# Optimization experiments

Measured on AMD Instinct MI355X. Metric: run time of the kernel, lower is better.

The kernel has to match this reference:

```python
import jax, jax.numpy as jnp
import numpy as np

D_MODEL = 1024
N_HEADS = 16
D_HEAD = D_MODEL // N_HEADS
N_INS = 3
RANK = 16
EPS = 1e-5


def gelu1p(x):
    # gelu1p feature map: 1 + GELU(x) (positive-ish feature map for linear attention)
    return 1.0 + jax.nn.gelu(x, approximate=False)


def setup_inputs() -> dict:
    key = jax.random.key(0)
    ks = jax.random.split(key, 16)
    B, T = 4, 8192
    x = jax.random.normal(ks[0], (B, T, D_MODEL), dtype=jnp.float32)
    pad_mask = jnp.ones((B, T), dtype=bool)
    s = 1.0 / np.sqrt(D_MODEL)
    wq = jax.random.normal(ks[1], (D_MODEL, D_MODEL), jnp.float32) * s
    wk = jax.random.normal(ks[2], (D_MODEL, D_MODEL), jnp.float32) * s
    wv = jax.random.normal(ks[3], (D_MODEL, D_MODEL), jnp.float32) * s
    wo = jax.random.normal(ks[4], (D_MODEL, D_MODEL), jnp.float32) * s
    sr = 1.0 / np.sqrt(RANK)
    # LoRA weights stacked over insertion points: down (n_ins, rank, d), up (n_ins, d, rank)
    # NOTE: original zero-inits 'up'; we use small random values so LoRA path is exercised.
    def lora(k1, k2):
        return (jax.random.normal(k1, (N_INS, RANK, D_MODEL), jnp.float32) * s,
                jax.random.normal(k2, (N_INS, D_MODEL, RANK), jnp.float32) * sr * 0.01)
    lqd, lqu = lora(ks[5], ks[6])
    lkd, lku = lora(ks[7], ks[8])
    lvd, lvu = lora(ks[9], ks[10])
    lod, lou = lora(ks[11], ks[12])
    return {"x": x, "pad_mask": pad_mask, "insertion_idx": 1,
            "wq": wq, "wk": wk, "wv": wv, "wo": wo,
            "lqd": lqd, "lqu": lqu, "lkd": lkd, "lku": lku,
            "lvd": lvd, "lvu": lvu, "lod": lod, "lou": lou}


def _proj(x, w, down, up):
    # base linear (no bias) + LoRA: x @ w.T + (x @ down.T) @ up.T
    return x @ w.T + (x @ down.T) @ up.T


def reference(x, pad_mask, insertion_idx, wq, wk, wv, wo,
              lqd, lqu, lkd, lku, lvd, lvu, lod, lou):
    B, T, D = x.shape
    i = insertion_idx
    q = _proj(x, wq, lqd[i], lqu[i])
    k = _proj(x, wk, lkd[i], lku[i])
    v = _proj(x, wv, lvd[i], lvu[i])
    # (B, T, H, dh) -> (B, H, T, dh)
    q = q.reshape(B, T, N_HEADS, D_HEAD).transpose(0, 2, 1, 3)
    k = k.reshape(B, T, N_HEADS, D_HEAD).transpose(0, 2, 1, 3)
    v = v.reshape(B, T, N_HEADS, D_HEAD).transpose(0, 2, 1, 3)
    q = gelu1p(q)
    k = gelu1p(k)
    m = pad_mask[:, None, :, None].astype(k.dtype)  # (B,1,T,1)
    k = k * m
    v = v * m
    context = jnp.einsum('bhtd,bhte->bhde', k, v)  # (B,H,dh,dh)
    z = k.sum(axis=-2)                              # (B,H,dh)
    num = jnp.einsum('bhtd,bhde->bhte', q, context)
    den = jnp.einsum('bhtd,bhd->bht', q, z)
    out = num / (den[..., None] + EPS)
    out = out.transpose(0, 2, 1, 3).reshape(B, T, D)
    out = _proj(out, wo, lod[i], lou[i])
    return out
```

## Files before the change

kernel.cpp:

```cpp
#include <hip/hip_runtime.h>
#include <hip/hip_bf16.h>

typedef unsigned short u16;
typedef __attribute__((ext_vector_type(8))) short short8;
typedef __attribute__((ext_vector_type(4))) float f32x4;
typedef __attribute__((ext_vector_type(4))) unsigned short us4;
typedef __attribute__((ext_vector_type(8))) unsigned short us8;

__device__ __forceinline__ u16 f2bf(float f) {
  unsigned int u = __float_as_uint(f);
  u += 0x7fffu + ((u >> 16) & 1u);
  return (u16)(u >> 16);
}
__device__ __forceinline__ float bf2f(u16 h) {
  return __uint_as_float(((unsigned int)h) << 16);
}
__device__ __forceinline__ float gelu1p_f(float x) {
  const float z  = x * 0.7071067811865475f;
  const float az = __builtin_fabsf(z);
  const float t  = __builtin_amdgcn_rcpf(__builtin_fmaf(0.3275911f, az, 1.0f));
  float pl = __builtin_fmaf(1.061405429f, t, -1.453152027f);
  pl = __builtin_fmaf(pl, t, 1.421413741f);
  pl = __builtin_fmaf(pl, t, -0.284496736f);
  pl = __builtin_fmaf(pl, t, 0.254829592f);
  pl = pl * t;
  const float e = __builtin_amdgcn_exp2f(-az * az * 1.4426950408889634f);
  float erfa = __builtin_fmaf(-pl, e, 1.0f);
  erfa = __builtin_copysignf(erfa, z);
  return __builtin_fmaf(x, 0.5f * (1.0f + erfa), 1.0f);
}
__device__ __forceinline__ void gll16(const void* g, void* l) {
  __builtin_amdgcn_global_load_lds(
      (const __attribute__((address_space(1))) unsigned int*)g,
      (__attribute__((address_space(3))) unsigned int*)l, 16, 0, 0);
}
#define FENCE() __builtin_amdgcn_sched_barrier(0)
#define BARRIER() __builtin_amdgcn_s_barrier()
#define LGKM0() do { asm volatile("s_waitcnt lgkmcnt(0)" ::: "memory"); FENCE(); } while (0)
#define VMCNT4() do { asm volatile("s_waitcnt vmcnt(4)" ::: "memory"); FENCE(); } while (0)
#define MFMA16(a, b, c) __builtin_amdgcn_mfma_f32_16x16x32_bf16(a, b, c, 0, 0, 0)

__global__ __launch_bounds__(256)
void build_weff(const float* __restrict__ wq, const float* __restrict__ wk,
                const float* __restrict__ wv, const float* __restrict__ wo,
                const float* __restrict__ lqd, const float* __restrict__ lqu,
                const float* __restrict__ lkd, const float* __restrict__ lku,
                const float* __restrict__ lvd, const float* __restrict__ lvu,
                const float* __restrict__ lod, const float* __restrict__ lou,
                const int* __restrict__ idxp,
                u16* __restrict__ wqkv, u16* __restrict__ wout) {
  const int blk = blockIdx.x;
  const int p = blk >> 10;
  const int n = blk & 1023;
  const int i = *idxp;
  const float* W  = (p == 0) ? wq  : (p == 1) ? wk  : (p == 2) ? wv  : wo;
  const float* Dn = ((p == 0) ? lqd : (p == 1) ? lkd : (p == 2) ? lvd : lod) + (size_t)i * 16 * 1024;
  const float* Up = ((p == 0) ? lqu : (p == 1) ? lku : (p == 2) ? lvu : lou) + (size_t)i * 1024 * 16;

  float up[16];
#pragma unroll
  for (int r = 0; r < 16; ++r) up[r] = Up[n * 16 + r];

  const int k0 = threadIdx.x << 2;
  f32x4 acc = *(const f32x4*)&W[(size_t)n * 1024 + k0];
#pragma unroll
  for (int r = 0; r < 16; ++r) {
    const f32x4 d = *(const f32x4*)&Dn[r * 1024 + k0];
#pragma unroll
    for (int j = 0; j < 4; ++j) acc[j] = __builtin_fmaf(up[r], d[j], acc[j]);
  }
  us4 o;
#pragma unroll
  for (int j = 0; j < 4; ++j) o[j] = f2bf(acc[j]);
  if (p < 3) *(us4*)&wqkv[(size_t)(p * 1024 + n) * 1024 + k0] = o;
  else       *(us4*)&wout[(size_t)n * 1024 + k0] = o;
}

__global__ void xcast(const float* __restrict__ x, u16* __restrict__ xb) {
  const size_t i = ((size_t)blockIdx.x * 256 + threadIdx.x) * 8;
  f32x4 a = *(const f32x4*)(x + i);
  f32x4 b = *(const f32x4*)(x + i + 4);
  us8 o;
#pragma unroll
  for (int j = 0; j < 4; ++j) { o[j] = f2bf(a[j]); o[j + 4] = f2bf(b[j]); }
  *(us8*)(xb + i) = o;
}

template <int MODE>
__global__ __launch_bounds__(512, 2)
void gemm8p(const u16* __restrict__ A, const u16* __restrict__ Bw,
            u16* __restrict__ qb, u16* __restrict__ kbuf, u16* __restrict__ vbuf,
            float* __restrict__ outf, const int* __restrict__ mask, int nbx) {
  const int nwg = gridDim.x;
  const int cpx = nwg >> 3;
  const int wg0 = blockIdx.x;
  const int swz = (wg0 & 7) * cpx + (wg0 >> 3);
  const int bx = swz % nbx;
  const int by = swz / nbx;
  const int row0 = by << 8, col0 = bx << 8;
  const int tid = threadIdx.x, lane = tid & 63, w = tid >> 6;
  const int wr = w >> 2, wc = w & 3;

  __shared__ __align__(16) u16 lds[2][2][2][8192];

  const int srow = (w << 4) + (lane & 15);
  const int scol = (lane >> 4) << 3;
  const u16* pA = A  + (size_t)(row0 + srow) * 1024 + scol;
  const u16* pB = Bw + (size_t)(col0 + srow) * 1024 + scol;

  auto stA = [&](int bb, int h, int ts) {
    const u16* s = pA + h * 131072 + ts * 64;
    u16* d = &lds[bb][0][h][((w << 7) + lane) << 3];
    gll16(s, d); gll16(s + 32, d + 512);
  };
  auto stB = [&](int bb, int h, int ts) {
    const u16* s = pB + h * 131072 + ts * 64;
    u16* d = &lds[bb][1][h][((w << 7) + lane) << 3];
    gll16(s, d); gll16(s + 32, d + 512);
  };
  auto LDA = [&](int bb, int m, int kk) {
    return *(const short8*)&lds[bb][0][wr][((((m << 1) | kk) << 6) | lane) << 3];
  };
  auto LDB = [&](int bb, int n, int kk) {
    const int nn = ((wc & 1) << 2) | n;
    return *(const short8*)&lds[bb][1][wc >> 1][((((nn << 1) | kk) << 6) | lane) << 3];
  };

  f32x4 acc[8][4] = {};
  short8 af[4][2], bfv[4][2];

  stA(0, 0, 0); stB(0, 0, 0); stA(0, 1, 0); stB(0, 1, 0);
  stB(1, 0, 1); stA(1, 0, 1);
  VMCNT4();
  BARRIER();

  auto tile = [&](int BUF, int t) {
    const int t1 = (t + 1 < 16) ? t + 1 : 15;
    const int t2 = (t + 2 < 16) ? t + 2 : 15;
#pragma unroll
    for (int m = 0; m < 4; ++m) { af[m][0] = LDA(BUF, m, 0); af[m][1] = LDA(BUF, m, 1); }
#pragma unroll
    for (int n = 0; n < 2; ++n) { bfv[n][0] = LDB(BUF, n, 0); bfv[n][1] = LDB(BUF, n, 1); }
    stA(BUF ^ 1, 1, t1);
    FENCE(); BARRIER(); LGKM0();
    __builtin_amdgcn_s_setprio(1);
#pragma unroll
    for (int m = 0; m < 4; ++m)
#pragma unroll
      for (int n = 0; n < 2; ++n) {
        acc[m][n] = MFMA16(af[m][0], bfv[n][0], acc[m][n]);
        acc[m][n] = MFMA16(af[m][1], bfv[n][1], acc[m][n]);
      }
    __builtin_amdgcn_s_setprio(0);
    FENCE(); BARRIER();
#pragma unroll
    for (int n = 2; n < 4; ++n) { bfv[n][0] = LDB(BUF, n, 0); bfv[n][1] = LDB(BUF, n, 1); }
    stB(BUF ^ 1, 1, t1);
    FENCE(); BARRIER(); LGKM0();
    __builtin_amdgcn_s_setprio(1);
#pragma unroll
    for (int m = 0; m < 4; ++m)
#pragma unroll
      for (int n = 2; n < 4; ++n) {
        acc[m][n] = MFMA16(af[m][0], bfv[n][0], acc[m][n]);
        acc[m][n] = MFMA16(af[m][1], bfv[n][1], acc[m][n]);
      }
    __builtin_amdgcn_s_setprio(0);
    FENCE(); BARRIER();
#pragma unroll
    for (int m = 0; m < 4; ++m) { af[m][0] = LDA(BUF, 4 + m, 0); af[m][1] = LDA(BUF, 4 + m, 1); }
    stB(BUF, 0, t2);
    FENCE(); BARRIER(); LGKM0();
    __builtin_amdgcn_s_setprio(1);
#pragma unroll
    for (int m = 0; m < 4; ++m)
#pragma unroll
      for (int n = 2; n < 4; ++n) {
        acc[4 + m][n] = MFMA16(af[m][0], bfv[n][0], acc[4 + m][n]);
        acc[4 + m][n] = MFMA16(af[m][1], bfv[n][1], acc[4 + m][n]);
      }
    __builtin_amdgcn_s_setprio(0);
    FENCE(); BARRIER();
    stA(BUF, 0, t2);
    FENCE(); BARRIER();
    __builtin_amdgcn_s_setprio(1);
#pragma unroll
    for (int m = 0; m < 4; ++m)
#pragma unroll
      for (int n = 0; n < 2; ++n) {
        acc[4 + m][n] = MFMA16(af[m][0], bfv[n][0], acc[4 + m][n]);
        acc[4 + m][n] = MFMA16(af[m][1], bfv[n][1], acc[4 + m][n]);
      }
    __builtin_amdgcn_s_setprio(0);
    FENCE();
    VMCNT4();
    BARRIER();
  };

#pragma unroll
  for (int it = 0; it < 8; ++it) { tile(0, 2 * it); tile(1, 2 * it + 1); }

  if (MODE == 0) {
    const int cw = col0 + (wc << 6);
    const int p = cw >> 10;
    u16* dst = (p == 0) ? qb : (p == 1) ? kbuf : vbuf;
    const int cc0 = (cw & 1023) + (lane & 15);
#pragma unroll
    for (int m = 0; m < 8; ++m) {
      const int r0 = row0 + (wr << 7) + (m << 4) + ((lane >> 4) << 2);
#pragma unroll
      for (int j = 0; j < 4; ++j) {
        const int r = r0 + j;
        const float mv = (p == 0) ? 1.0f : ((mask[r] != 0) ? 1.0f : 0.0f);
#pragma unroll
        for (int n = 0; n < 4; ++n) {
          float v = acc[m][n][j];
          v = (p == 2) ? v * mv : gelu1p_f(v) * mv;
          dst[(size_t)r * 1024 + cc0 + (n << 4)] = f2bf(v);
        }
      }
    }
  } else {
    const int c0 = col0 + (wc << 6) + (lane & 15);
#pragma unroll
    for (int m = 0; m < 8; ++m) {
      const int r0 = row0 + (wr << 7) + (m << 4) + ((lane >> 4) << 2);
#pragma unroll
      for (int n = 0; n < 4; ++n)
#pragma unroll
        for (int j = 0; j < 4; ++j)
          outf[(size_t)(r0 + j) * 1024 + c0 + (n << 4)] = acc[m][n][j];
    }
  }
}

__global__ __launch_bounds__(64)
void ctx_mfma(const u16* __restrict__ kbuf, const u16* __restrict__ vbuf,
              float* __restrict__ Cpart, float* __restrict__ zpart) {
  const int lane = threadIdx.x;
  const int bh = blockIdx.y, sl = blockIdx.x;
  const int b = bh >> 4, h = bh & 15;
  const size_t base = ((size_t)b * 8192 + (size_t)sl * 512) * 1024 + h * 64;
  const int colA = lane & 15;
  const int tj0 = (lane >> 4) << 3;

  short8 ones;
#pragma unroll
  for (int j = 0; j < 8; ++j) ones[j] = (short)0x3F80;

  f32x4 acc[4][5] = {};

  for (int c = 0; c < 16; ++c) {
    const size_t tbase = base + (size_t)(c * 32 + tj0) * 1024;
    short8 af[4], bv[4];
#pragma unroll
    for (int s = 0; s < 4; ++s) {
      const u16* pk = kbuf + tbase + s * 16 + colA;
      const u16* pv = vbuf + tbase + s * 16 + colA;
      short8 a, v;
#pragma unroll
      for (int j = 0; j < 8; ++j) { a[j] = (short)pk[j * 1024]; v[j] = (short)pv[j * 1024]; }
      af[s] = a; bv[s] = v;
    }
#pragma unroll
    for (int di = 0; di < 4; ++di) {
#pragma unroll
      for (int ei = 0; ei < 4; ++ei)
        acc[di][ei] = MFMA16(af[di], bv[ei], acc[di][ei]);
      acc[di][4] = MFMA16(af[di], ones, acc[di][4]);
    }
  }

  float* cp = Cpart + (size_t)(bh * 16 + sl) * 4096;
  const int el = lane & 15, rb = (lane >> 4) << 2;
#pragma unroll
  for (int di = 0; di < 4; ++di)
#pragma unroll
    for (int j = 0; j < 4; ++j) {
      const int d = di * 16 + rb + j;
#pragma unroll
      for (int ei = 0; ei < 4; ++ei)
        cp[d * 64 + ei * 16 + el] = acc[di][ei][j];
    }
  if (el == 0) {
    float* zp = zpart + (size_t)(bh * 16 + sl) * 64;
#pragma unroll
    for (int di = 0; di < 4; ++di)
#pragma unroll
      for (int j = 0; j < 4; ++j) zp[di * 16 + rb + j] = acc[di][4][j];
  }
}

__global__ void ctx_reduce(const float* __restrict__ Cpart, const float* __restrict__ zpart,
                           u16* __restrict__ Cb) {
  const int bh = blockIdx.x, tid = threadIdx.x;
  for (int idx = tid; idx < 5120; idx += 256) {
    const int d = idx / 80;
    const int e = idx - d * 80;
    float s = 0.f;
    if (e < 64) {
#pragma unroll
      for (int c = 0; c < 16; ++c) s += Cpart[(size_t)(bh * 16 + c) * 4096 + d * 64 + e];
    } else if (e == 64) {
#pragma unroll
      for (int c = 0; c < 16; ++c) s += zpart[(size_t)(bh * 16 + c) * 64 + d];
    }
    Cb[(size_t)bh * 5120 + idx] = f2bf(s);
  }
}

__global__ __launch_bounds__(256)
void attn_out(const u16* __restrict__ qbuf, const u16* __restrict__ Cb,
              u16* __restrict__ ratio) {
  const int tid = threadIdx.x, lane = tid & 63, wave = tid >> 6;
  const int bh = blockIdx.y, b = bh >> 4, h = bh & 15;
  const int t0 = blockIdx.x * 256 + wave * 64;
  const size_t mbase = (size_t)b * 8192;
  const u16* cb = Cb + (size_t)bh * 5120;

  short8 bfrag[5][2];
#pragma unroll
  for (int nt = 0; nt < 5; ++nt)
#pragma unroll
    for (int kf = 0; kf < 2; ++kf) {
      short8 f;
#pragma unroll
      for (int j = 0; j < 8; ++j) {
        const int d = kf * 32 + ((lane >> 4) << 3) + j;
        f[j] = (short)cb[d * 80 + nt * 16 + (lane & 15)];
      }
      bfrag[nt][kf] = f;
    }

  f32x4 acc[4][5] = {};
#pragma unroll
  for (int mt = 0; mt < 4; ++mt) {
    const int tr = t0 + mt * 16 + (lane & 15);
    const u16* qrow = qbuf + (mbase + tr) * 1024 + h * 64 + ((lane >> 4) << 3);
    short8 a0 = *(const short8*)qrow;
    short8 a1 = *(const short8*)(qrow + 32);
#pragma unroll
    for (int nt = 0; nt < 5; ++nt) {
      acc[mt][nt] = MFMA16(a0, bfrag[nt][0], acc[mt][nt]);
      acc[mt][nt] = MFMA16(a1, bfrag[nt][1], acc[mt][nt]);
    }
  }

#pragma unroll
  for (int mt = 0; mt < 4; ++mt) {
#pragma unroll
    for (int j = 0; j < 4; ++j) {
      const float den = __shfl(acc[mt][4][j], lane & 48, 64);
      const float inv = 1.0f / (den + 1e-5f);
      const int tr = t0 + mt * 16 + ((lane >> 4) << 2) + j;
      u16* orow = ratio + (mbase + tr) * 1024 + h * 64;
#pragma unroll
      for (int nt = 0; nt < 4; ++nt)
        orow[nt * 16 + (lane & 15)] = f2bf(acc[mt][nt][j] * inv);
    }
  }
}

extern "C" void kernel_launch(void* const* d_in, const int* in_sizes, int n_in,
                              void* d_out, int out_size, void* d_ws, size_t ws_size,
                              hipStream_t stream) {
  (void)in_sizes; (void)n_in; (void)out_size; (void)ws_size;
  const float* x = (const float*)d_in[0];
  const int* mask = (const int*)d_in[1];
  const int* idx = (const int*)d_in[2];
  const float* wq = (const float*)d_in[3];
  const float* wk = (const float*)d_in[4];
  const float* wv = (const float*)d_in[5];
  const float* wo = (const float*)d_in[6];
  const float* lqd = (const float*)d_in[7];
  const float* lqu = (const float*)d_in[8];
  const float* lkd = (const float*)d_in[9];
  const float* lku = (const float*)d_in[10];
  const float* lvd = (const float*)d_in[11];
  const float* lvu = (const float*)d_in[12];
  const float* lod = (const float*)d_in[13];
  const float* lou = (const float*)d_in[14];
  float* out = (float*)d_out;

  char* ws = (char*)d_ws;
  u16* xb    = (u16*)ws;
  u16* wqkv  = (u16*)(ws + (64ll << 20));
  u16* wo_b  = (u16*)(ws + (70ll << 20));
  u16* qb    = (u16*)(ws + (72ll << 20));
  u16* kb    = (u16*)(ws + (136ll << 20));
  u16* vb    = (u16*)(ws + (200ll << 20));
  float* Cpart = (float*)ws;
  float* zpart = (float*)(ws + (272ll << 20));
  u16* Cb    = (u16*)(ws + (273ll << 20));
  u16* ratio = xb;

  build_weff<<<dim3(4096), dim3(256), 0, stream>>>(wq, wk, wv, wo,
      lqd, lqu, lkd, lku, lvd, lvu, lod, lou, idx, wqkv, wo_b);
  xcast<<<dim3(16384), dim3(256), 0, stream>>>(x, xb);
  gemm8p<0><<<dim3(1536), dim3(512), 0, stream>>>(xb, wqkv, qb, kb, vb, nullptr, mask, 12);
  ctx_mfma<<<dim3(16, 64), dim3(64), 0, stream>>>(kb, vb, Cpart, zpart);
  ctx_reduce<<<dim3(64), dim3(256), 0, stream>>>(Cpart, zpart, Cb);
  attn_out<<<dim3(32, 64), dim3(256), 0, stream>>>(qb, Cb, ratio);
  gemm8p<1><<<dim3(512), dim3(512), 0, stream>>>(ratio, wo_b, nullptr, nullptr, nullptr, out, mask, 4);
}
```

Baseline: 491.1 us.

## Shrink GEMM tiles to 128x128 with four-wave workgroups

Replaces the 256x256-tile, 8-wave GEMM with a 128x128-tile, 4-wave variant that restages its loads, LDS layout and MFMA phase schedule, and quadruples the grid. It is meant to raise occupancy and wave-level parallelism and to cut tail effects on the smaller output GEMM. In exchange, each tile does less arithmetic per byte loaded, so global/L2 traffic per FLOP roughly doubles. It also adds a vmcnt(0) wait before the epilogue.

```diff
diff --git a/kernel.cpp b/kernel.cpp
--- a/kernel.cpp
+++ b/kernel.cpp
@@ -38,6 +38,7 @@
 #define BARRIER() __builtin_amdgcn_s_barrier()
 #define LGKM0() do { asm volatile("s_waitcnt lgkmcnt(0)" ::: "memory"); FENCE(); } while (0)
 #define VMCNT4() do { asm volatile("s_waitcnt vmcnt(4)" ::: "memory"); FENCE(); } while (0)
+#define VMCNT0() do { asm volatile("s_waitcnt vmcnt(0)" ::: "memory"); FENCE(); } while (0)
 #define MFMA16(a, b, c) __builtin_amdgcn_mfma_f32_16x16x32_bf16(a, b, c, 0, 0, 0)
 
 __global__ __launch_bounds__(256)
@@ -87,8 +88,8 @@
 }
 
 template <int MODE>
-__global__ __launch_bounds__(512, 2)
-void gemm8p(const u16* __restrict__ A, const u16* __restrict__ Bw,
+__global__ __launch_bounds__(256, 2)
+void gemm4w(const u16* __restrict__ A, const u16* __restrict__ Bw,
             u16* __restrict__ qb, u16* __restrict__ kbuf, u16* __restrict__ vbuf,
             float* __restrict__ outf, const int* __restrict__ mask, int nbx) {
   const int nwg = gridDim.x;
@@ -97,40 +98,39 @@
   const int swz = (wg0 & 7) * cpx + (wg0 >> 3);
   const int bx = swz % nbx;
   const int by = swz / nbx;
-  const int row0 = by << 8, col0 = bx << 8;
+  const int row0 = by << 7, col0 = bx << 7;
   const int tid = threadIdx.x, lane = tid & 63, w = tid >> 6;
-  const int wr = w >> 2, wc = w & 3;
-
-  __shared__ __align__(16) u16 lds[2][2][2][8192];
-
-  const int srow = (w << 4) + (lane & 15);
-  const int scol = (lane >> 4) << 3;
-  const u16* pA = A  + (size_t)(row0 + srow) * 1024 + scol;
-  const u16* pB = Bw + (size_t)(col0 + srow) * 1024 + scol;
-
-  auto stA = [&](int bb, int h, int ts) {
-    const u16* s = pA + h * 131072 + ts * 64;
-    u16* d = &lds[bb][0][h][((w << 7) + lane) << 3];
-    gll16(s, d); gll16(s + 32, d + 512);
+  const int wr = w >> 1, wc = w & 1;
+
+  __shared__ __align__(16) u16 lds[2][2][2][4096];
+
+  int goff[2];
+#pragma unroll
+  for (int c = 0; c < 2; ++c) {
+    const int sub = c * 256 + tid;
+    goff[c] = ((sub >> 7) * 16 + (sub & 15)) * 1024 + ((sub >> 6) & 1) * 32 + ((sub >> 4) & 3) * 8;
+  }
+  const u16* pA = A  + (size_t)row0 * 1024;
+  const u16* pB = Bw + (size_t)col0 * 1024;
+
+  auto stage = [&](int bb, int mat, int h, int ts) {
+    const u16* base = (mat == 0 ? pA : pB) + h * 65536 + ts * 64;
+#pragma unroll
+    for (int c = 0; c < 2; ++c)
+      gll16(base + goff[c], &lds[bb][mat][h][(c * 256 + tid) * 8]);
   };
-  auto stB = [&](int bb, int h, int ts) {
-    const u16* s = pB + h * 131072 + ts * 64;
-    u16* d = &lds[bb][1][h][((w << 7) + lane) << 3];
-    gll16(s, d); gll16(s + 32, d + 512);
+  auto LDA = [&](int bb, int mt, int kk) {
+    return *(const short8*)&lds[bb][0][wr][((((mt << 1) | kk) << 6) | lane) << 3];
   };
-  auto LDA = [&](int bb, int m, int kk) {
-    return *(const short8*)&lds[bb][0][wr][((((m << 1) | kk) << 6) | lane) << 3];
+  auto LDB = [&](int bb, int nt, int kk) {
+    return *(const short8*)&lds[bb][1][wc][((((nt << 1) | kk) << 6) | lane) << 3];
   };
-  auto LDB = [&](int bb, int n, int kk) {
-    const int nn = ((wc & 1) << 2) | n;
-    return *(const short8*)&lds[bb][1][wc >> 1][((((nn << 1) | kk) << 6) | lane) << 3];
-  };
-
-  f32x4 acc[8][4] = {};
+
+  f32x4 acc[4][4] = {};
   short8 af[4][2], bfv[4][2];
 
-  stA(0, 0, 0); stB(0, 0, 0); stA(0, 1, 0); stB(0, 1, 0);
-  stB(1, 0, 1); stA(1, 0, 1);
+  stage(0, 0, 0, 0); stage(0, 1, 0, 0); stage(0, 0, 1, 0); stage(0, 1, 1, 0);
+  stage(1, 0, 0, 1); stage(1, 1, 0, 1);
   VMCNT4();
   BARRIER();
 
@@ -138,14 +138,14 @@
     const int t1 = (t + 1 < 16) ? t + 1 : 15;
     const int t2 = (t + 2 < 16) ? t + 2 : 15;
 #pragma unroll
-    for (int m = 0; m < 4; ++m) { af[m][0] = LDA(BUF, m, 0); af[m][1] = LDA(BUF, m, 1); }
+    for (int m = 0; m < 2; ++m) { af[m][0] = LDA(BUF, m, 0); af[m][1] = LDA(BUF, m, 1); }
 #pragma unroll
     for (int n = 0; n < 2; ++n) { bfv[n][0] = LDB(BUF, n, 0); bfv[n][1] = LDB(BUF, n, 1); }
-    stA(BUF ^ 1, 1, t1);
+    stage(BUF ^ 1, 0, 1, t1);
     FENCE(); BARRIER(); LGKM0();
     __builtin_amdgcn_s_setprio(1);
 #pragma unroll
-    for (int m = 0; m < 4; ++m)
+    for (int m = 0; m < 2; ++m)
 #pragma unroll
       for (int n = 0; n < 2; ++n) {
         acc[m][n] = MFMA16(af[m][0], bfv[n][0], acc[m][n]);
@@ -154,12 +154,25 @@
     __builtin_amdgcn_s_setprio(0);
     FENCE(); BARRIER();
 #pragma unroll
-    for (int n = 2; n < 4; ++n) { bfv[n][0] = LDB(BUF, n, 0); bfv[n][1] = LDB(BUF, n, 1); }
-    stB(BUF ^ 1, 1, t1);
+    for (int m = 2; m < 4; ++m) { af[m][0] = LDA(BUF, m, 0); af[m][1] = LDA(BUF, m, 1); }
+    stage(BUF ^ 1, 1, 1, t1);
     FENCE(); BARRIER(); LGKM0();
     __builtin_amdgcn_s_setprio(1);
 #pragma unroll
-    for (int m = 0; m < 4; ++m)
+    for (int m = 2; m < 4; ++m)
+#pragma unroll
+      for (int n = 0; n < 2; ++n) {
+        acc[m][n] = MFMA16(af[m][0], bfv[n][0], acc[m][n]);
+        acc[m][n] = MFMA16(af[m][1], bfv[n][1], acc[m][n]);
+      }
+    __builtin_amdgcn_s_setprio(0);
+    FENCE(); BARRIER();
+#pragma unroll
+    for (int n = 2; n < 4; ++n) { bfv[n][0] = LDB(BUF, n, 0); bfv[n][1] = LDB(BUF, n, 1); }
+    FENCE(); BARRIER(); LGKM0();
+    __builtin_amdgcn_s_setprio(1);
+#pragma unroll
+    for (int m = 2; m < 4; ++m)
 #pragma unroll
       for (int n = 2; n < 4; ++n) {
         acc[m][n] = MFMA16(af[m][0], bfv[n][0], acc[m][n]);
@@ -167,29 +180,15 @@
       }
     __builtin_amdgcn_s_setprio(0);
     FENCE(); BARRIER();
-#pragma unroll
-    for (int m = 0; m < 4; ++m) { af[m][0] = LDA(BUF, 4 + m, 0); af[m][1] = LDA(BUF, 4 + m, 1); }
-    stB(BUF, 0, t2);
-    FENCE(); BARRIER(); LGKM0();
+    stage(BUF, 0, 0, t2); stage(BUF, 1, 0, t2);
+    FENCE();
     __builtin_amdgcn_s_setprio(1);
 #pragma unroll
-    for (int m = 0; m < 4; ++m)
+    for (int m = 0; m < 2; ++m)
 #pragma unroll
       for (int n = 2; n < 4; ++n) {
-        acc[4 + m][n] = MFMA16(af[m][0], bfv[n][0], acc[4 + m][n]);
-        acc[4 + m][n] = MFMA16(af[m][1], bfv[n][1], acc[4 + m][n]);
-      }
-    __builtin_amdgcn_s_setprio(0);
-    FENCE(); BARRIER();
-    stA(BUF, 0, t2);
-    FENCE(); BARRIER();
-    __builtin_amdgcn_s_setprio(1);
-#pragma unroll
-    for (int m = 0; m < 4; ++m)
-#pragma unroll
-      for (int n = 0; n < 2; ++n) {
-        acc[4 + m][n] = MFMA16(af[m][0], bfv[n][0], acc[4 + m][n]);
-        acc[4 + m][n] = MFMA16(af[m][1], bfv[n][1], acc[4 + m][n]);
+        acc[m][n] = MFMA16(af[m][0], bfv[n][0], acc[m][n]);
+        acc[m][n] = MFMA16(af[m][1], bfv[n][1], acc[m][n]);
       }
     __builtin_amdgcn_s_setprio(0);
     FENCE();
@@ -199,15 +198,15 @@
 
 #pragma unroll
   for (int it = 0; it < 8; ++it) { tile(0, 2 * it); tile(1, 2 * it + 1); }
+  VMCNT0();
 
   if (MODE == 0) {
-    const int cw = col0 + (wc << 6);
-    const int p = cw >> 10;
+    const int p = col0 >> 10;
     u16* dst = (p == 0) ? qb : (p == 1) ? kbuf : vbuf;
-    const int cc0 = (cw & 1023) + (lane & 15);
-#pragma unroll
-    for (int m = 0; m < 8; ++m) {
-      const int r0 = row0 + (wr << 7) + (m << 4) + ((lane >> 4) << 2);
+    const int cc0 = (col0 & 1023) + (wc << 6) + (lane & 15);
+#pragma unroll
+    for (int m = 0; m < 4; ++m) {
+      const int r0 = row0 + (wr << 6) + (m << 4) + ((lane >> 4) << 2);
 #pragma unroll
       for (int j = 0; j < 4; ++j) {
         const int r = r0 + j;
@@ -223,8 +222,8 @@
   } else {
     const int c0 = col0 + (wc << 6) + (lane & 15);
 #pragma unroll
-    for (int m = 0; m < 8; ++m) {
-      const int r0 = row0 + (wr << 7) + (m << 4) + ((lane >> 4) << 2);
+    for (int m = 0; m < 4; ++m) {
+      const int r0 = row0 + (wr << 6) + (m << 4) + ((lane >> 4) << 2);
 #pragma unroll
       for (int n = 0; n < 4; ++n)
 #pragma unroll
@@ -397,9 +396,9 @@
   build_weff<<<dim3(4096), dim3(256), 0, stream>>>(wq, wk, wv, wo,
       lqd, lqu, lkd, lku, lvd, lvu, lod, lou, idx, wqkv, wo_b);
   xcast<<<dim3(16384), dim3(256), 0, stream>>>(x, xb);
-  gemm8p<0><<<dim3(1536), dim3(512), 0, stream>>>(xb, wqkv, qb, kb, vb, nullptr, mask, 12);
+  gemm4w<0><<<dim3(6144), dim3(256), 0, stream>>>(xb, wqkv, qb, kb, vb, nullptr, mask, 24);
   ctx_mfma<<<dim3(16, 64), dim3(64), 0, stream>>>(kb, vb, Cpart, zpart);
   ctx_reduce<<<dim3(64), dim3(256), 0, stream>>>(Cpart, zpart, Cb);
   attn_out<<<dim3(32, 64), dim3(256), 0, stream>>>(qb, Cb, ratio);
-  gemm8p<1><<<dim3(512), dim3(512), 0, stream>>>(ratio, wo_b, nullptr, nullptr, nullptr, out, mask, 4);
-}
+  gemm4w<1><<<dim3(2048), dim3(256), 0, stream>>>(ratio, wo_b, nullptr, nullptr, nullptr, out, mask, 8);
+}
```

New measurement: 700.8 us. +42.7%, slower.
